# Kernel tuning notes

Hardware: AMD Instinct MI355X
Metric: run time of the kernel (lower is better)

## Reference

```python
import jax, jax.numpy as jnp
import numpy as np

B, LQ, LA, D, H = 8, 2048, 2048, 300, 150

def setup_inputs() -> dict:
    key = jax.random.key(0)
    ks = jax.random.split(key, 6)
    return {
        "Q": jax.random.normal(ks[0], (B, LQ, D), dtype=jnp.float32),
        "A": jax.random.normal(ks[1], (B, LA, D), dtype=jnp.float32),
        "Wi": jax.random.normal(ks[2], (D, H), dtype=jnp.float32) * (1.0 / np.sqrt(D)),
        "Wu": jax.random.normal(ks[3], (D, H), dtype=jnp.float32) * (1.0 / np.sqrt(D)),
        "Wg": jax.random.normal(ks[4], (H, H), dtype=jnp.float32) * (1.0 / np.sqrt(H)),
        "Wt": jax.random.normal(ks[5], (2 * H, H), dtype=jnp.float32) * (1.0 / np.sqrt(2 * H)),
        "bi": jnp.zeros((H,), dtype=jnp.float32),
        "bu": jnp.zeros((H,), dtype=jnp.float32),
        "bg": jnp.zeros((H,), dtype=jnp.float32),
        "bt": jnp.zeros((H,), dtype=jnp.float32),
    }

def reference(Q, A, Wi, Wu, Wg, Wt, bi, bu, bg, bt):
    # sigmoid/tanh gated projections (shared weights for Q and A)
    def gate(X):
        return jax.nn.sigmoid(X @ Wi + bi) * jnp.tanh(X @ Wu + bu)
    Qh = gate(Q)  # [B, LQ, H]
    Ah = gate(A)  # [B, LA, H]
    # attention scores G[b,q,a] = <(Qh Wg + bg)[b,q], Ah[b,a]>
    G = jnp.einsum('bqh,bah->bqa', Qh @ Wg + bg, Ah)
    G = jax.nn.softmax(G, axis=1)  # softmax over Q positions
    # H[b,a] = sum_q G[b,q,a] * Qh[b,q]
    Hm = jnp.einsum('bqa,bqh->bah', G, Qh)  # [B, LA, H]
    # 'nn' comparison: relu(concat([Ah, Hm]) @ Wt + bt)
    T = jax.nn.relu(jnp.concatenate([Ah, Hm], axis=-1) @ Wt + bt)
    return T
```

## Files before the change

### kernel.cpp

```cpp
#include <hip/hip_runtime.h>
#include <math.h>

#define BB 8
#define LQ 2048
#define DD 300
#define HHH 150
#define NROWS (BB * LQ)

#define KP 168
#define QTS 72
#define WCE 27136
#define SLAB_B 45056
#define SLAB_E 22528
#define QHT_OFF_E 11008

typedef __bf16 bf16x8 __attribute__((ext_vector_type(8)));
typedef __bf16 bf16x4 __attribute__((ext_vector_type(4)));
typedef float f32x16 __attribute__((ext_vector_type(16)));

__device__ __forceinline__ void gl_lds16(const void* g, void* l) {
    __builtin_amdgcn_global_load_lds(
        (const __attribute__((address_space(1))) void*)g,
        (__attribute__((address_space(3))) void*)l,
        16, 0, 0);
}
__device__ __forceinline__ void stage_flat(const void* g, void* l, int bytes,
                                           int w, int lane) {
    for (int ofs = w * 1024; ofs < bytes; ofs += 4096)
        gl_lds16((const char*)g + ofs + lane * 16, (char*)l + ofs);
}
__device__ __forceinline__ void stage_flat8(const void* g, void* l, int bytes,
                                            int w, int lane) {
    for (int ofs = w * 1024; ofs < bytes; ofs += 8192)
        gl_lds16((const char*)g + ofs + lane * 16, (char*)l + ofs);
}
__device__ __forceinline__ f32x16 z16() {
    f32x16 v;
#pragma unroll
    for (int i = 0; i < 16; i++) v[i] = 0.f;
    return v;
}
__device__ __forceinline__ bf16x8 cvt8(float4 u, float4 v) {
    return (bf16x8){(__bf16)u.x, (__bf16)u.y, (__bf16)u.z, (__bf16)u.w,
                    (__bf16)v.x, (__bf16)v.y, (__bf16)v.z, (__bf16)v.w};
}

__global__ __launch_bounds__(256) void convert_weights(
    const float* __restrict__ Wi, const float* __restrict__ Wu,
    const float* __restrict__ Wg, const float* __restrict__ Wt,
    __bf16* __restrict__ WiC, __bf16* __restrict__ WuC,
    __bf16* __restrict__ WgT, __bf16* __restrict__ Wt12)
{
    const int z = blockIdx.y;
    const int i = blockIdx.x * 256 + threadIdx.x;
    if (z < 2) {
        if (i >= 2 * WCE) return;
        int c = i / WCE, rem = i - c * WCE;
        float v = 0.f;
        if (rem < 160 * KP) {
            int h = rem / KP, kc = rem - h * KP;
            int d = c * 160 + kc;
            if (kc < 160 && d < DD && h < HHH) v = (z ? Wu : Wi)[(size_t)d * HHH + h];
        }
        (z ? WuC : WiC)[i] = (__bf16)v;
    } else if (z == 2) {
        if (i >= WCE) return;
        float v = 0.f;
        if (i < 160 * KP) {
            int h = i / KP, kc = i - h * KP;
            if (kc < HHH && h < HHH) v = Wg[(size_t)kc * HHH + h];
        }
        WgT[i] = (__bf16)v;
    } else {
        if (i >= 2 * 160 * KP) return;
        int c = i / (160 * KP), rem = i - c * (160 * KP);
        int h = rem / KP, kc = rem - h * KP;
        float v = (kc < HHH && h < HHH) ? Wt[(size_t)(c * HHH + kc) * HHH + h] : 0.f;
        Wt12[i] = (__bf16)v;
    }
}

__global__ __launch_bounds__(512, 2) void gatep(
    const float* __restrict__ Q, const float* __restrict__ A,
    const __bf16* __restrict__ WiC, const __bf16* __restrict__ WuC,
    const __bf16* __restrict__ WgT,
    const float* __restrict__ bi, const float* __restrict__ bu,
    const float* __restrict__ bg,
    __bf16* __restrict__ AhB, __bf16* __restrict__ Slab)
{
    __shared__ __align__(16) __bf16 WB[2][WCE];
    __shared__ __align__(16) __bf16 QhA[128 * KP];
    const int tid = threadIdx.x;
    const int w = tid >> 6, lane = tid & 63;
    const int m32 = lane & 31, half = lane >> 5;
    const int wm = w & 3, wn = w >> 2;
    const int tof = wn ? 3 : 0, tn = wn ? 2 : 3;
    const int z = blockIdx.y;
    const int r0 = blockIdx.x * 128;
    const float* X = z ? A : Q;

    stage_flat8(WiC, WB[0], 54272, w, lane);

    const float* xrow = X + (size_t)(r0 + wm * 32 + m32) * DD + half * 8;
    bf16x8 af0[10], af1[10];
#pragma unroll
    for (int ks = 0; ks < 10; ks++) {
        float4 u = *(const float4*)(xrow + ks * 16);
        float4 v = *(const float4*)(xrow + ks * 16 + 4);
        af0[ks] = cvt8(u, v);
    }

    f32x16 ai[3], au[3];
#pragma unroll
    for (int t = 0; t < 3; t++) { ai[t] = z16(); au[t] = z16(); }

    __syncthreads();
    stage_flat8(WuC, WB[1], 54272, w, lane);

#pragma unroll
    for (int ks = 0; ks < 8; ks++) {
        float4 u = *(const float4*)(xrow + 160 + ks * 16);
        float4 v = *(const float4*)(xrow + 160 + ks * 16 + 4);
        af1[ks] = cvt8(u, v);
    }
    {
        float4 u = *(const float4*)(xrow + 288);
        float4 v = (half == 0) ? *(const float4*)(xrow + 292) : (float4){0.f, 0.f, 0.f, 0.f};
        af1[8] = cvt8(u, v);
        af1[9] = (bf16x8){(__bf16)0.f, (__bf16)0.f, (__bf16)0.f, (__bf16)0.f,
                          (__bf16)0.f, (__bf16)0.f, (__bf16)0.f, (__bf16)0.f};
    }

    for (int ks = 0; ks < 10; ks++)
#pragma unroll
        for (int ti = 0; ti < 3; ti++)
            if (ti < tn)
                ai[ti] = __builtin_amdgcn_mfma_f32_32x32x16_bf16(
                    af0[ks], *(const bf16x8*)(WB[0] + ((tof + ti) * 32 + m32) * KP + ks * 16 + half * 8),
                    ai[ti], 0, 0, 0);
    __syncthreads();
    stage_flat8(WiC + WCE, WB[0], 54272, w, lane);
    for (int ks = 0; ks < 10; ks++)
#pragma unroll
        for (int ti = 0; ti < 3; ti++)
            if (ti < tn)
                au[ti] = __builtin_amdgcn_mfma_f32_32x32x16_bf16(
                    af0[ks], *(const bf16x8*)(WB[1] + ((tof + ti) * 32 + m32) * KP + ks * 16 + half * 8),
                    au[ti], 0, 0, 0);
    __syncthreads();
    stage_flat8(WuC + WCE, WB[1], 54272, w, lane);
    for (int ks = 0; ks < 10; ks++)
#pragma unroll
        for (int ti = 0; ti < 3; ti++)
            if (ti < tn)
                ai[ti] = __builtin_amdgcn_mfma_f32_32x32x16_bf16(
                    af1[ks], *(const bf16x8*)(WB[0] + ((tof + ti) * 32 + m32) * KP + ks * 16 + half * 8),
                    ai[ti], 0, 0, 0);
    __syncthreads();
    if (z == 0) stage_flat8(WgT, WB[0], 54272, w, lane);
    for (int ks = 0; ks < 10; ks++)
#pragma unroll
        for (int ti = 0; ti < 3; ti++)
            if (ti < tn)
                au[ti] = __builtin_amdgcn_mfma_f32_32x32x16_bf16(
                    af1[ks], *(const bf16x8*)(WB[1] + ((tof + ti) * 32 + m32) * KP + ks * 16 + half * 8),
                    au[ti], 0, 0, 0);

#pragma unroll
    for (int ti = 0; ti < 3; ti++) {
        if (ti >= tn) continue;
        int h = (tof + ti) * 32 + m32;
        int hc = h < HHH ? h : 0;
        float bih = bi[hc], buh = bu[hc];
#pragma unroll
        for (int r = 0; r < 16; r++) {
            float v = 0.f;
            if (h < HHH) {
                float xi = ai[ti][r] + bih, xu = au[ti][r] + buh;
                float s = 1.f / (1.f + __expf(-xi));
                float tt = 1.f - 2.f / (1.f + __expf(2.f * xu));
                v = s * tt;
            }
            ai[ti][r] = v;
        }
    }

    if (z) {
#pragma unroll
        for (int ti = 0; ti < 3; ti++) {
            if (ti >= tn) continue;
            int h = (tof + ti) * 32 + m32;
#pragma unroll
            for (int r = 0; r < 16; r++) {
                int rowp = (r & 3) + 8 * (r >> 2) + 4 * half;
                AhB[(size_t)(r0 + wm * 32 + rowp) * KP + h] = (__bf16)ai[ti][r];
            }
        }
        return;
    }

#pragma unroll
    for (int ti = 0; ti < 3; ti++) {
        if (ti >= tn) continue;
        int h = (tof + ti) * 32 + m32;
#pragma unroll
        for (int r = 0; r < 16; r++) {
            int rowp = (r & 3) + 8 * (r >> 2) + 4 * half;
            QhA[(wm * 32 + rowp) * KP + h] = (__bf16)ai[ti][r];
        }
    }
    __syncthreads();

    bf16x8 afq[10];
#pragma unroll
    for (int ks = 0; ks < 10; ks++)
        afq[ks] = *(const bf16x8*)(QhA + (wm * 32 + m32) * KP + ks * 16 + half * 8);

    f32x16 qg[3];
#pragma unroll
    for (int t = 0; t < 3; t++) qg[t] = z16();
    for (int ks = 0; ks < 10; ks++)
#pragma unroll
        for (int ti = 0; ti < 3; ti++)
            if (ti < tn)
                qg[ti] = __builtin_amdgcn_mfma_f32_32x32x16_bf16(
                    afq[ks], *(const bf16x8*)(WB[0] + ((tof + ti) * 32 + m32) * KP + ks * 16 + half * 8),
                    qg[ti], 0, 0, 0);

    const int b = r0 >> 11, qt0 = (r0 & 2047) >> 6;
#pragma unroll
    for (int ti = 0; ti < 3; ti++) {
        if (ti >= tn) continue;
        int h = (tof + ti) * 32 + m32;
        int hc = h < HHH ? h : 0;
        float bgh = bg[hc];
#pragma unroll
        for (int r = 0; r < 16; r++) {
            int rowp = (r & 3) + 8 * (r >> 2) + 4 * half;
            int q = (r0 & 2047) + wm * 32 + rowp;
            float v = (h < HHH) ? (qg[ti][r] + bgh) : 0.f;
            Slab[(size_t)(b * 32 + (q >> 6)) * SLAB_E + (q & 63) * KP + h] = (__bf16)v;
        }
    }

    {
        const int jl = tid & 63, tile = (tid >> 6) & 1, hgrp = tid >> 7;
        for (int hseg = hgrp; hseg < 20; hseg += 4) {
            bf16x8 vv = *(const bf16x8*)(QhA + (tile * 64 + jl) * KP + hseg * 8);
            __bf16* dst = Slab + (size_t)(b * 32 + qt0 + tile) * SLAB_E + QHT_OFF_E + jl;
#pragma unroll
            for (int e = 0; e < 8; e++)
                dst[(hseg * 8 + e) * QTS] = vv[e];
        }
    }
}

__global__ __launch_bounds__(512, 2) void attn_mfma(
    const __bf16* __restrict__ Slab, const __bf16* __restrict__ AhB,
    __bf16* __restrict__ O, float* __restrict__ L)
{
    __shared__ __align__(16) __bf16 Buf[2][SLAB_E];
    __shared__ __align__(16) __bf16 PS[256 * QTS];
    const int tid = threadIdx.x;
    const int w = tid >> 6, lane = tid & 63;
    const int m32 = lane & 31, half = lane >> 5;
    const int grp = blockIdx.x;
    const int b = grp >> 2, qp = grp & 3;
    const int a0 = blockIdx.y * 256;

    const char* slabBase = (const char*)Slab + (size_t)(b * 32 + qp * 8) * SLAB_B;
    stage_flat8(slabBase, Buf[0], SLAB_B, w, lane);

    const __bf16* arow = AhB + (size_t)(b * LQ + a0 + w * 32 + m32) * KP + half * 8;
    bf16x8 af[10];
#pragma unroll
    for (int ks = 0; ks < 10; ks++)
        af[ks] = *(const bf16x8*)(arow + ks * 16);

    float lsum[16];
#pragma unroll
    for (int r = 0; r < 16; r++) lsum[r] = 0.f;
    f32x16 acc[5];
#pragma unroll
    for (int t = 0; t < 5; t++) acc[t] = z16();
    __syncthreads();

    for (int qt = 0; qt < 8; qt++) {
        const int cur = qt & 1;
        if (qt < 7)
            stage_flat8(slabBase + (size_t)(qt + 1) * SLAB_B, Buf[cur ^ 1], SLAB_B, w, lane);
        const __bf16* Bq = Buf[cur];
        const __bf16* Bv = Buf[cur] + QHT_OFF_E;

        f32x16 s0 = z16(), s1 = z16();
        for (int ks = 0; ks < 10; ks++) {
            bf16x8 b0 = *(const bf16x8*)(Bq + m32 * KP + ks * 16 + half * 8);
            bf16x8 b1 = *(const bf16x8*)(Bq + (32 + m32) * KP + ks * 16 + half * 8);
            s0 = __builtin_amdgcn_mfma_f32_32x32x16_bf16(af[ks], b0, s0, 0, 0, 0);
            s1 = __builtin_amdgcn_mfma_f32_32x32x16_bf16(af[ks], b1, s1, 0, 0, 0);
        }

#pragma unroll
        for (int r = 0; r < 16; r++) {
            int rowp = (r & 3) + 8 * (r >> 2) + 4 * half;
            float p0 = __expf(s0[r]);
            float p1 = __expf(s1[r]);
            PS[(w * 32 + rowp) * QTS + m32] = (__bf16)p0;
            PS[(w * 32 + rowp) * QTS + 32 + m32] = (__bf16)p1;
            lsum[r] += p0 + p1;
        }

#pragma unroll
        for (int kk = 0; kk < 4; kk++) {
            bf16x8 pf = *(const bf16x8*)(PS + (w * 32 + m32) * QTS + kk * 16 + half * 8);
#pragma unroll
            for (int t = 0; t < 5; t++)
                acc[t] = __builtin_amdgcn_mfma_f32_32x32x16_bf16(
                    pf, *(const bf16x8*)(Bv + (t * 32 + m32) * QTS + kk * 16 + half * 8),
                    acc[t], 0, 0, 0);
        }
        __syncthreads();
    }

#pragma unroll
    for (int r = 0; r < 16; r++) {
        float s = lsum[r];
#pragma unroll
        for (int m = 1; m < 32; m <<= 1) s += __shfl_xor(s, m, 64);
        lsum[r] = s;
    }
    __bf16* Ob = O + ((size_t)qp * NROWS + b * LQ + a0 + w * 32) * 160;
#pragma unroll
    for (int t = 0; t < 5; t++) {
        int h = t * 32 + m32;
#pragma unroll
        for (int r = 0; r < 16; r++) {
            int rowp = (r & 3) + 8 * (r >> 2) + 4 * half;
            Ob[(size_t)rowp * 160 + h] = (__bf16)acc[t][r];
        }
    }
    if (m32 == 0) {
        float* Lb = L + (size_t)qp * NROWS + b * LQ + a0 + w * 32;
#pragma unroll
        for (int r = 0; r < 16; r++) {
            int rowp = (r & 3) + 8 * (r >> 2) + 4 * half;
            Lb[rowp] = lsum[r];
        }
    }
}

__global__ __launch_bounds__(256, 1) void final_mfma(
    const __bf16* __restrict__ AhB, const __bf16* __restrict__ O,
    const float* __restrict__ L, const __bf16* __restrict__ Wt12,
    const float* __restrict__ bt, float* __restrict__ Out)
{
    __shared__ __align__(16) __bf16 AS[64 * KP];
    __shared__ __align__(16) __bf16 HS[64 * KP];
    __shared__ __align__(16) __bf16 WtS[2 * 160 * KP];
    const int tid = threadIdx.x;
    const int w = tid >> 6, lane = tid & 63;
    const int m32 = lane & 31, half = lane >> 5;
    const int r0 = blockIdx.x * 64;

    stage_flat(AhB + (size_t)r0 * KP, AS, 21504, w, lane);
    stage_flat(Wt12, WtS, 107520, w, lane);

    {
        int rhat = tid >> 2, qq = tid & 3;
        int grow = r0 + rhat;
        float inv = 1.f / (L[grow] + L[NROWS + grow] + L[2 * NROWS + grow] + L[3 * NROWS + grow]);
#pragma unroll
        for (int k = 0; k < 5; k++) {
            float sum[8];
#pragma unroll
            for (int j = 0; j < 8; j++) sum[j] = 0.f;
#pragma unroll
            for (int p = 0; p < 4; p++) {
                bf16x8 x = *(const bf16x8*)(O + ((size_t)p * NROWS + grow) * 160 + qq * 40 + k * 8);
#pragma unroll
                for (int j = 0; j < 8; j++) sum[j] += (float)x[j];
            }
            bf16x8 hv;
#pragma unroll
            for (int j = 0; j < 8; j++) hv[j] = (__bf16)(sum[j] * inv);
            *(bf16x8*)(HS + rhat * KP + qq * 40 + k * 8) = hv;
        }
    }
    __syncthreads();

    const int m = w & 1, th = w >> 1;
    const int tbase = th ? 3 : 0, tn = th ? 2 : 3;
    f32x16 acc[3];
#pragma unroll
    for (int i = 0; i < 3; i++) acc[i] = z16();

    for (int ch = 0; ch < 2; ch++) {
        const __bf16* src = ch ? HS : AS;
        for (int ks = 0; ks < 10; ks++) {
            bf16x8 af = *(const bf16x8*)(src + (m * 32 + m32) * KP + ks * 16 + half * 8);
#pragma unroll
            for (int ti = 0; ti < 3; ti++) {
                if (ti < tn) {
                    int t = tbase + ti;
                    acc[ti] = __builtin_amdgcn_mfma_f32_32x32x16_bf16(
                        af, *(const bf16x8*)(WtS + (ch * 160 + t * 32 + m32) * KP + ks * 16 + half * 8),
                        acc[ti], 0, 0, 0);
                }
            }
        }
    }

#pragma unroll
    for (int ti = 0; ti < 3; ti++) {
        if (ti < tn) {
            int t = tbase + ti;
            int h = t * 32 + m32;
            if (h < HHH) {
                float bth = bt[h];
#pragma unroll
                for (int r = 0; r < 16; r++) {
                    int rowp = (r & 3) + 8 * (r >> 2) + 4 * half;
                    float v = acc[ti][r] + bth;
                    Out[(size_t)(r0 + m * 32 + rowp) * HHH + h] = v > 0.f ? v : 0.f;
                }
            }
        }
    }
}

extern "C" void kernel_launch(void* const* d_in, const int* in_sizes, int n_in,
                              void* d_out, int out_size, void* d_ws, size_t ws_size,
                              hipStream_t stream)
{
    const float* Q  = (const float*)d_in[0];
    const float* A  = (const float*)d_in[1];
    const float* Wi = (const float*)d_in[2];
    const float* Wu = (const float*)d_in[3];
    const float* Wg = (const float*)d_in[4];
    const float* Wt = (const float*)d_in[5];
    const float* bi = (const float*)d_in[6];
    const float* bu = (const float*)d_in[7];
    const float* bg = (const float*)d_in[8];
    const float* bt = (const float*)d_in[9];
    float* out = (float*)d_out;

    char* ws = (char*)d_ws;
    __bf16* Slab = (__bf16*)(ws);
    __bf16* AhB  = (__bf16*)(ws + 11534336);
    __bf16* Op   = (__bf16*)(ws + 17039360);
    float*  Lp   = (float*) (ws + 38010880);
    __bf16* WiC  = (__bf16*)(ws + 38273024);
    __bf16* WuC  = (__bf16*)(ws + 38381568);
    __bf16* WgT  = (__bf16*)(ws + 38490112);
    __bf16* Wt12 = (__bf16*)(ws + 38544384);

    convert_weights<<<dim3(212, 4), 256, 0, stream>>>(Wi, Wu, Wg, Wt,
                                                      WiC, WuC, WgT, Wt12);
    gatep<<<dim3(NROWS / 128, 2), 512, 0, stream>>>(Q, A, WiC, WuC, WgT,
                                                    bi, bu, bg, AhB, Slab);
    attn_mfma<<<dim3(32, 8), 512, 0, stream>>>(Slab, AhB, Op, Lp);
    final_mfma<<<NROWS / 64, 256, 0, stream>>>(AhB, Op, Lp, Wt12, bt, out);
}
```

Baseline: 158.0 us.

## Keep softmax probabilities in registers via transposed MFMA and permlane swap

The attention kernel swaps the MFMA operand order so the score accumulator comes out transposed. Each lane can then pack its exp values straight into bf16 A-fragments with v_cvt_pk_bf16_f32 and v_permlane32_swap, which removes the LDS round trip through the PS buffer and frees that shared memory. The row sum shrinks to one scalar per lane, the output store becomes vectorized bf16x4 writes, and the final-iteration barrier and MFMA priority hints are tuned. The cost is reliance on gfx950-specific instructions and a correct fragment mapping, which would silently produce wrong results if the layout is off.

```diff
diff --git a/kernel.cpp b/kernel.cpp
--- a/kernel.cpp
+++ b/kernel.cpp
@@ -43,6 +43,19 @@
 __device__ __forceinline__ bf16x8 cvt8(float4 u, float4 v) {
     return (bf16x8){(__bf16)u.x, (__bf16)u.y, (__bf16)u.z, (__bf16)u.w,
                     (__bf16)v.x, (__bf16)v.y, (__bf16)v.z, (__bf16)v.w};
+}
+__device__ __forceinline__ unsigned pk2(float lo, float hi) {
+    unsigned d;
+    asm("v_cvt_pk_bf16_f32 %0, %1, %2" : "=v"(d) : "v"(lo), "v"(hi));
+    return d;
+}
+__device__ __forceinline__ void pl32(unsigned& a, unsigned& b) {
+    asm("v_permlane32_swap_b32 %0, %1" : "+v"(a), "+v"(b));
+}
+__device__ __forceinline__ bf16x8 mk8(unsigned a, unsigned b, unsigned c, unsigned d) {
+    union { unsigned u[4]; bf16x8 v; } x;
+    x.u[0] = a; x.u[1] = b; x.u[2] = c; x.u[3] = d;
+    return x.v;
 }
 
 __global__ __launch_bounds__(256) void convert_weights(
@@ -260,7 +273,6 @@
     __bf16* __restrict__ O, float* __restrict__ L)
 {
     __shared__ __align__(16) __bf16 Buf[2][SLAB_E];
-    __shared__ __align__(16) __bf16 PS[256 * QTS];
     const int tid = threadIdx.x;
     const int w = tid >> 6, lane = tid & 63;
     const int m32 = lane & 31, half = lane >> 5;
@@ -277,9 +289,7 @@
     for (int ks = 0; ks < 10; ks++)
         af[ks] = *(const bf16x8*)(arow + ks * 16);
 
-    float lsum[16];
-#pragma unroll
-    for (int r = 0; r < 16; r++) lsum[r] = 0.f;
+    float lsum = 0.f;
     f32x16 acc[5];
 #pragma unroll
     for (int t = 0; t < 5; t++) acc[t] = z16();
@@ -293,60 +303,67 @@
         const __bf16* Bv = Buf[cur] + QHT_OFF_E;
 
         f32x16 s0 = z16(), s1 = z16();
+        __builtin_amdgcn_s_setprio(1);
         for (int ks = 0; ks < 10; ks++) {
             bf16x8 b0 = *(const bf16x8*)(Bq + m32 * KP + ks * 16 + half * 8);
             bf16x8 b1 = *(const bf16x8*)(Bq + (32 + m32) * KP + ks * 16 + half * 8);
-            s0 = __builtin_amdgcn_mfma_f32_32x32x16_bf16(af[ks], b0, s0, 0, 0, 0);
-            s1 = __builtin_amdgcn_mfma_f32_32x32x16_bf16(af[ks], b1, s1, 0, 0, 0);
-        }
-
-#pragma unroll
-        for (int r = 0; r < 16; r++) {
-            int rowp = (r & 3) + 8 * (r >> 2) + 4 * half;
-            float p0 = __expf(s0[r]);
-            float p1 = __expf(s1[r]);
-            PS[(w * 32 + rowp) * QTS + m32] = (__bf16)p0;
-            PS[(w * 32 + rowp) * QTS + 32 + m32] = (__bf16)p1;
-            lsum[r] += p0 + p1;
-        }
-
-#pragma unroll
-        for (int kk = 0; kk < 4; kk++) {
-            bf16x8 pf = *(const bf16x8*)(PS + (w * 32 + m32) * QTS + kk * 16 + half * 8);
+            s0 = __builtin_amdgcn_mfma_f32_32x32x16_bf16(b0, af[ks], s0, 0, 0, 0);
+            s1 = __builtin_amdgcn_mfma_f32_32x32x16_bf16(b1, af[ks], s1, 0, 0, 0);
+        }
+        __builtin_amdgcn_s_setprio(0);
+
+#pragma unroll
+        for (int r = 0; r < 16; r++) { s0[r] = __expf(s0[r]); lsum += s0[r]; }
+#pragma unroll
+        for (int r = 0; r < 16; r++) { s1[r] = __expf(s1[r]); lsum += s1[r]; }
+
+        bf16x8 pf[4];
+        {
+            unsigned w01 = pk2(s0[0], s0[1]),   w45 = pk2(s0[4], s0[5]);
+            unsigned w23 = pk2(s0[2], s0[3]),   w67 = pk2(s0[6], s0[7]);
+            pl32(w01, w45); pl32(w23, w67);
+            pf[0] = mk8(w01, w23, w45, w67);
+            unsigned x01 = pk2(s0[8], s0[9]),   x45 = pk2(s0[12], s0[13]);
+            unsigned x23 = pk2(s0[10], s0[11]), x67 = pk2(s0[14], s0[15]);
+            pl32(x01, x45); pl32(x23, x67);
+            pf[1] = mk8(x01, x23, x45, x67);
+        }
+        {
+            unsigned w01 = pk2(s1[0], s1[1]),   w45 = pk2(s1[4], s1[5]);
+            unsigned w23 = pk2(s1[2], s1[3]),   w67 = pk2(s1[6], s1[7]);
+            pl32(w01, w45); pl32(w23, w67);
+            pf[2] = mk8(w01, w23, w45, w67);
+            unsigned x01 = pk2(s1[8], s1[9]),   x45 = pk2(s1[12], s1[13]);
+            unsigned x23 = pk2(s1[10], s1[11]), x67 = pk2(s1[14], s1[15]);
+            pl32(x01, x45); pl32(x23, x67);
+            pf[3] = mk8(x01, x23, x45, x67);
+        }
+
+        __builtin_amdgcn_s_setprio(1);
+#pragma unroll
+        for (int kk = 0; kk < 4; kk++)
 #pragma unroll
             for (int t = 0; t < 5; t++)
                 acc[t] = __builtin_amdgcn_mfma_f32_32x32x16_bf16(
-                    pf, *(const bf16x8*)(Bv + (t * 32 + m32) * QTS + kk * 16 + half * 8),
-                    acc[t], 0, 0, 0);
-        }
-        __syncthreads();
-    }
-
-#pragma unroll
-    for (int r = 0; r < 16; r++) {
-        float s = lsum[r];
-#pragma unroll
-        for (int m = 1; m < 32; m <<= 1) s += __shfl_xor(s, m, 64);
-        lsum[r] = s;
-    }
+                    *(const bf16x8*)(Bv + (t * 32 + m32) * QTS + kk * 16 + half * 8),
+                    pf[kk], acc[t], 0, 0, 0);
+        __builtin_amdgcn_s_setprio(0);
+        if (qt < 7) __syncthreads();
+    }
+
+    float lt = lsum + __shfl_xor(lsum, 32, 64);
+
     __bf16* Ob = O + ((size_t)qp * NROWS + b * LQ + a0 + w * 32) * 160;
 #pragma unroll
-    for (int t = 0; t < 5; t++) {
-        int h = t * 32 + m32;
-#pragma unroll
-        for (int r = 0; r < 16; r++) {
-            int rowp = (r & 3) + 8 * (r >> 2) + 4 * half;
-            Ob[(size_t)rowp * 160 + h] = (__bf16)acc[t][r];
-        }
-    }
-    if (m32 == 0) {
-        float* Lb = L + (size_t)qp * NROWS + b * LQ + a0 + w * 32;
-#pragma unroll
-        for (int r = 0; r < 16; r++) {
-            int rowp = (r & 3) + 8 * (r >> 2) + 4 * half;
-            Lb[rowp] = lsum[r];
-        }
-    }
+    for (int t = 0; t < 5; t++)
+#pragma unroll
+        for (int rq = 0; rq < 4; rq++) {
+            bf16x4 hv = {(__bf16)acc[t][rq * 4 + 0], (__bf16)acc[t][rq * 4 + 1],
+                         (__bf16)acc[t][rq * 4 + 2], (__bf16)acc[t][rq * 4 + 3]};
+            *(bf16x4*)(Ob + (size_t)m32 * 160 + t * 32 + rq * 8 + half * 4) = hv;
+        }
+    if (half == 0)
+        L[(size_t)qp * NROWS + b * LQ + a0 + w * 32 + m32] = lt;
 }
 
 __global__ __launch_bounds__(256, 1) void final_mfma(
```

After: 159.6 us. About the same (+1.0%).
